# Performance work log

Measured on AMD Instinct MI355X. Metric: run time of the kernel, lower is better.

Reference implementation:

```python
import jax, jax.numpy as jnp
import numpy as np

T = 5       # Newton-Schulz iterations
EPS = 1e-5


def setup_inputs() -> dict:
    key = jax.random.key(0)
    k1, k2 = jax.random.split(key)
    N, F = 500000, 128
    X = jax.random.normal(k1, (N, F), dtype=jnp.float32)
    # running_rot buffer: random orthogonal rotation (eye at init; use QR for a non-trivial one)
    M = jax.random.normal(k2, (1, F, F), dtype=jnp.float32)
    Q, _ = jnp.linalg.qr(M)
    return {"X": X, "running_rot": Q.astype(jnp.float32)}


def _whiten(X):
    # iterative_normalization_py.forward, training path, g=1 group
    x = X.T[None]                              # [g=1, d, m]
    d, m = x.shape[1], x.shape[2]
    mean = jnp.mean(x, axis=-1, keepdims=True)
    xc = x - mean                              # centered [1, d, m]
    I = jnp.eye(d, dtype=X.dtype)[None]
    # Sigma = eps*I + xc xc^T / m  (baddbmm with beta=eps, alpha=1/m)
    Sigma = EPS * I + jnp.einsum('gdm,gem->gde', xc, xc) / m
    rTr = 1.0 / jnp.trace(Sigma, axis1=1, axis2=2)[:, None, None]  # 1/tr(Sigma)
    Sn = Sigma * rTr                           # trace-normalized covariance
    P = I
    for _ in range(T):                         # P_{k+1} = 1.5 P_k - 0.5 P_k^3 Sn
        P = 1.5 * P - 0.5 * (P @ P @ P @ Sn)
    wm = P * jnp.sqrt(rTr)                     # whitening matrix = Sigma^{-1/2} (approx)
    xn = wm @ xc                               # [1, d, m]
    return xn[0].T                             # back to [N, F]


def reference(X, running_rot):
    Xn = _whiten(X)                            # [N, F]
    # X_hat = einsum('bgc,gdc->bgd', X_hat, running_rot) with g=1
    out = jnp.einsum('nc,dc->nd', Xn, running_rot[0])
    return out
```

## Files before the change

### kernel.cpp

```cpp
#include <hip/hip_runtime.h>
#include <math.h>

#define NROWS  500000
#define NCHK   7813
#define EPSV   1e-5f

typedef __bf16 bf16_t;
typedef __bf16 bf16x4 __attribute__((ext_vector_type(4)));
typedef __bf16 bf16x8 __attribute__((ext_vector_type(8)));
typedef float  f32x4  __attribute__((ext_vector_type(4)));

static const size_t GT_OFF   = 131072;
static const size_t WB_OFF   = 327680;
static const size_t MEAN_OFF = 360448;
static const size_t BIAS_OFF = 360960;
static const size_t CS_OFF   = 393216;
static const size_t GRAM_OFF = 1048576;

__global__ __launch_bounds__(256) void k_stats(const float* __restrict__ X,
        float* __restrict__ csPart, float* __restrict__ gramPart) {
    __shared__ bf16_t sxtT[2][8192];
    __shared__ float  scs[256][4];
    const int t    = threadIdx.x;
    const int lane = t & 63;
    const int w    = t >> 6;
    const int oct  = t >> 5;
    const int fg4  = t & 31;
    const int cl   = lane & 15;
    const int kq   = lane >> 4;
    const int G    = gridDim.x;

    f32x4 acc[2][8];
    #pragma unroll
    for (int a = 0; a < 2; a++)
        #pragma unroll
        for (int b = 0; b < 8; b++)
            acc[a][b] = (f32x4){0.f, 0.f, 0.f, 0.f};
    float cs0 = 0.f, cs1 = 0.f, cs2 = 0.f, cs3 = 0.f;

    f32x4 R[8];

    auto KF = [](int f) { return (f ^ (f >> 3)) & 7; };

    auto GLOADC = [&](int ch) {
        const size_t row0 = (size_t)ch << 6;
        #pragma unroll
        for (int i = 0; i < 8; i++) {
            const size_t row = row0 + oct * 8 + i;
            R[i] = (row < NROWS)
                 ? *reinterpret_cast<const f32x4*>(X + row * 128 + fg4 * 4)
                 : (f32x4){0.f, 0.f, 0.f, 0.f};
        }
    };
    auto DSWRITEC = [&](int buf) {
        #pragma unroll
        for (int i = 0; i < 8; i++) {
            cs0 += R[i][0]; cs1 += R[i][1]; cs2 += R[i][2]; cs3 += R[i][3];
        }
        bf16_t* S = sxtT[buf];
        #pragma unroll
        for (int j = 0; j < 4; j++) {
            const int f = fg4 * 4 + j;
            const int g = oct ^ KF(f);
            bf16x8 v;
            #pragma unroll
            for (int i = 0; i < 8; i++) v[i] = (bf16_t)R[i][j];
            *reinterpret_cast<bf16x8*>(&S[f * 64 + g * 8]) = v;
        }
    };
    auto MFMAC = [&](int buf) {
        const bf16_t* S = sxtT[buf];
        #pragma unroll
        for (int kb = 0; kb < 2; kb++) {
            const int gq = kb * 4 + kq;
            bf16x8 fa[2];
            #pragma unroll
            for (int a = 0; a < 2; a++) {
                const int f = (w * 2 + a) * 16 + cl;
                fa[a] = *reinterpret_cast<const bf16x8*>(&S[f * 64 + ((gq ^ KF(f)) << 3)]);
            }
            #pragma unroll
            for (int b = 0; b < 8; b++) {
                const int f = b * 16 + cl;
                const bf16x8 fb = *reinterpret_cast<const bf16x8*>(&S[f * 64 + ((gq ^ KF(f)) << 3)]);
                acc[0][b] = __builtin_amdgcn_mfma_f32_16x16x32_bf16(fa[0], fb, acc[0][b], 0, 0, 0);
                acc[1][b] = __builtin_amdgcn_mfma_f32_16x16x32_bf16(fa[1], fb, acc[1][b], 0, 0, 0);
            }
        }
    };

    int ch0 = blockIdx.x;
    GLOADC(ch0);
    DSWRITEC(0);
    __syncthreads();
    for (;;) {
        const int ch1 = ch0 + G;
        const bool v1 = ch1 < NCHK;
        if (v1) GLOADC(ch1);
        MFMAC(0);
        if (v1) DSWRITEC(1);
        __syncthreads();
        if (!v1) break;
        const int ch2 = ch1 + G;
        const bool v2 = ch2 < NCHK;
        if (v2) GLOADC(ch2);
        MFMAC(1);
        if (v2) DSWRITEC(0);
        __syncthreads();
        if (!v2) break;
        ch0 = ch2;
    }

    float* gp = gramPart + (size_t)blockIdx.x * 16384;
    #pragma unroll
    for (int a = 0; a < 2; a++)
        #pragma unroll
        for (int b = 0; b < 8; b++) {
            const int col  = b * 16 + cl;
            const int row0 = (w * 2 + a) * 16 + kq * 4;
            __builtin_nontemporal_store(acc[a][b],
                reinterpret_cast<f32x4*>(&gp[col * 128 + row0]));
        }
    scs[t][0] = cs0; scs[t][1] = cs1; scs[t][2] = cs2; scs[t][3] = cs3;
    __syncthreads();
    if (t < 128) {
        float s = 0.f;
        #pragma unroll
        for (int q = 0; q < 8; q++) s += scs[q * 32 + (t >> 2)][t & 3];
        csPart[(size_t)blockIdx.x * 128 + t] = s;
    }
}

__global__ __launch_bounds__(256) void k_gred(const float* __restrict__ gramPart,
        const float* __restrict__ csPart, float* __restrict__ gramTot,
        float* __restrict__ mean, int G) {
    const int t = threadIdx.x;
    const int b = blockIdx.x;
    if (b == 256) {
        if (t < 128) {
            float s = 0.f;
            int g = 0;
            for (; g + 8 <= G; g += 8) {
                float p[8];
                #pragma unroll
                for (int u = 0; u < 8; u++) p[u] = csPart[(size_t)(g + u) * 128 + t];
                s += ((p[0] + p[1]) + (p[2] + p[3])) + ((p[4] + p[5]) + (p[6] + p[7]));
            }
            for (; g < G; g++) s += csPart[(size_t)g * 128 + t];
            mean[t] = s * (1.0f / (float)NROWS);
        }
        return;
    }
    const int e  = b * 64 + (t & 63);
    const int sl = t >> 6;
    float s = 0.f;
    int g = sl;
    for (; g + 28 < G; g += 32) {
        float v[8];
        #pragma unroll
        for (int u = 0; u < 8; u++)
            v[u] = __builtin_nontemporal_load(&gramPart[(size_t)(g + 4 * u) * 16384 + e]);
        s += ((v[0] + v[1]) + (v[2] + v[3])) + ((v[4] + v[5]) + (v[6] + v[7]));
    }
    for (; g < G; g += 4)
        s += __builtin_nontemporal_load(&gramPart[(size_t)g * 16384 + e]);
    __shared__ float red[4][64];
    red[sl][t & 63] = s;
    __syncthreads();
    if (t < 64)
        gramTot[b * 64 + t] = (red[0][t] + red[1][t]) + (red[2][t] + red[3][t]);
}

__global__ __launch_bounds__(256) void k_ns(const float* __restrict__ gramTot,
        const float* __restrict__ mean, const float* __restrict__ Rg,
        bf16_t* __restrict__ Wb, float* __restrict__ bias) {
    __shared__ bf16_t sPh[16384], sPl[16384], sSn[16384], sTT[16384];
    const int t = threadIdx.x;
    const int w = t >> 6, lane = t & 63;
    const int cl = lane & 15, kq = lane >> 4;

    float* rs = reinterpret_cast<float*>(sTT);
    float dv = 0.f;
    if (t < 128) {
        const float m = mean[t];
        dv = gramTot[t * 129] * (1.0f / (float)NROWS) - m * m + EPSV;
    }
    rs[t] = dv;
    __syncthreads();
    #pragma unroll
    for (int off = 128; off > 0; off >>= 1) {
        if (t < off) rs[t] += rs[t + off];
        __syncthreads();
    }
    const float rTr = 1.0f / rs[0];
    __syncthreads();
    for (int i = 0; i < 64; i++) {
        const int e = t + (i << 8);
        const int r = e >> 7, c = e & 127;
        float s = gramTot[e] * (1.0f / (float)NROWS) - mean[r] * mean[c];
        if (r == c) s += EPSV;
        const int ix = r * 128 + (c ^ ((r & 7) << 3));
        const float snv = s * rTr;
        sSn[ix] = (bf16_t)snv;
        const float p0 = ((r == c) ? 1.5f : 0.f) - 0.5f * snv;
        const bf16_t ph = (bf16_t)p0;
        sPh[ix] = ph;
        sPl[ix] = (bf16_t)(p0 - (float)ph);
    }
    __syncthreads();

    f32x4 acc[2][8];
    auto NSMM = [&](const bf16_t* __restrict__ Bm) {
        #pragma unroll
        for (int a = 0; a < 2; a++)
            #pragma unroll
            for (int ct = 0; ct < 8; ct++) acc[a][ct] = (f32x4){0.f, 0.f, 0.f, 0.f};
        #pragma unroll
        for (int kb = 0; kb < 4; kb++) {
            const int k0 = kb * 32 + kq * 8;
            bf16x8 ah[2], al[2];
            #pragma unroll
            for (int a = 0; a < 2; a++) {
                const int ra = w * 32 + a * 16 + cl;
                const int ia = ra * 128 + (k0 ^ ((ra & 7) << 3));
                ah[a] = *reinterpret_cast<const bf16x8*>(&sPh[ia]);
                al[a] = *reinterpret_cast<const bf16x8*>(&sPl[ia]);
            }
            #pragma unroll
            for (int ct = 0; ct < 8; ct++) {
                const int rb = ct * 16 + cl;
                const bf16x8 bb = *reinterpret_cast<const bf16x8*>(
                    &Bm[rb * 128 + (k0 ^ ((rb & 7) << 3))]);
                acc[0][ct] = __builtin_amdgcn_mfma_f32_16x16x32_bf16(ah[0], bb, acc[0][ct], 0, 0, 0);
                acc[0][ct] = __builtin_amdgcn_mfma_f32_16x16x32_bf16(al[0], bb, acc[0][ct], 0, 0, 0);
                acc[1][ct] = __builtin_amdgcn_mfma_f32_16x16x32_bf16(ah[1], bb, acc[1][ct], 0, 0, 0);
                acc[1][ct] = __builtin_amdgcn_mfma_f32_16x16x32_bf16(al[1], bb, acc[1][ct], 0, 0, 0);
            }
        }
    };
    auto WRT = [&](bf16_t* __restrict__ D) {
        #pragma unroll
        for (int a = 0; a < 2; a++) {
            const int ro0 = w * 32 + a * 16 + kq * 4;
            #pragma unroll
            for (int ct = 0; ct < 8; ct++) {
                const int co = ct * 16 + cl;
                bf16x4 v = { (bf16_t)acc[a][ct][0], (bf16_t)acc[a][ct][1],
                             (bf16_t)acc[a][ct][2], (bf16_t)acc[a][ct][3] };
                *reinterpret_cast<bf16x4*>(&D[co * 128 + (ro0 ^ ((co & 7) << 3))]) = v;
            }
        }
    };

    for (int it = 0; it < 4; it++) {
        NSMM(sSn);
        WRT(sTT);
        __syncthreads();
        NSMM(sTT);
        __syncthreads();
        WRT(sTT);
        __syncthreads();
        NSMM(sTT);
        #pragma unroll
        for (int a = 0; a < 2; a++) {
            const int ro0 = w * 32 + a * 16 + kq * 4;
            #pragma unroll
            for (int ct = 0; ct < 8; ct++) {
                const int co = ct * 16 + cl;
                const int ix = co * 128 + (ro0 ^ ((co & 7) << 3));
                bf16x4 ph4 = *reinterpret_cast<const bf16x4*>(&sPh[ix]);
                bf16x4 pl4 = *reinterpret_cast<const bf16x4*>(&sPl[ix]);
                bf16x4 nh, nl;
                #pragma unroll
                for (int r = 0; r < 4; r++) {
                    const float pold = (float)ph4[r] + (float)pl4[r];
                    const float pn = 1.5f * pold - 0.5f * acc[a][ct][r];
                    nh[r] = (bf16_t)pn;
                    nl[r] = (bf16_t)(pn - (float)nh[r]);
                }
                *reinterpret_cast<bf16x4*>(&sPh[ix]) = nh;
                *reinterpret_cast<bf16x4*>(&sPl[ix]) = nl;
            }
        }
        __syncthreads();
    }

    const float scal = sqrtf(rTr);
    #pragma unroll
    for (int a = 0; a < 2; a++)
        #pragma unroll
        for (int ct = 0; ct < 8; ct++) acc[a][ct] = (f32x4){0.f, 0.f, 0.f, 0.f};
    #pragma unroll
    for (int kb = 0; kb < 4; kb++) {
        const int k0 = kb * 32 + kq * 8;
        bf16x8 ah[2], al[2];
        #pragma unroll
        for (int a = 0; a < 2; a++) {
            const int ra = w * 32 + a * 16 + cl;
            const float4 rv0 = *reinterpret_cast<const float4*>(&Rg[ra * 128 + k0]);
            const float4 rv1 = *reinterpret_cast<const float4*>(&Rg[ra * 128 + k0 + 4]);
            const float rv[8] = {rv0.x, rv0.y, rv0.z, rv0.w, rv1.x, rv1.y, rv1.z, rv1.w};
            bf16x8 h, l;
            #pragma unroll
            for (int j = 0; j < 8; j++) {
                h[j] = (bf16_t)rv[j];
                l[j] = (bf16_t)(rv[j] - (float)h[j]);
            }
            ah[a] = h; al[a] = l;
        }
        #pragma unroll
        for (int ct = 0; ct < 8; ct++) {
            const int rb = ct * 16 + cl;
            const int ib = rb * 128 + (k0 ^ ((rb & 7) << 3));
            const bf16x8 bh = *reinterpret_cast<const bf16x8*>(&sPh[ib]);
            const bf16x8 bl = *reinterpret_cast<const bf16x8*>(&sPl[ib]);
            #pragma unroll
            for (int a = 0; a < 2; a++) {
                acc[a][ct] = __builtin_amdgcn_mfma_f32_16x16x32_bf16(ah[a], bh, acc[a][ct], 0, 0, 0);
                acc[a][ct] = __builtin_amdgcn_mfma_f32_16x16x32_bf16(al[a], bh, acc[a][ct], 0, 0, 0);
                acc[a][ct] = __builtin_amdgcn_mfma_f32_16x16x32_bf16(ah[a], bl, acc[a][ct], 0, 0, 0);
            }
        }
    }
    #pragma unroll
    for (int a = 0; a < 2; a++) {
        float pb[4] = {0.f, 0.f, 0.f, 0.f};
        #pragma unroll
        for (int ct = 0; ct < 8; ct++) {
            const float mv = mean[ct * 16 + cl];
            #pragma unroll
            for (int r = 0; r < 4; r++) {
                const float wv = acc[a][ct][r] * scal;
                Wb[(w * 32 + a * 16 + kq * 4 + r) * 128 + ct * 16 + cl] = (bf16_t)wv;
                pb[r] += wv * mv;
            }
        }
        #pragma unroll
        for (int r = 0; r < 4; r++) {
            float v = pb[r];
            v += __shfl_xor(v, 1);
            v += __shfl_xor(v, 2);
            v += __shfl_xor(v, 4);
            v += __shfl_xor(v, 8);
            if (cl == 0) bias[w * 32 + a * 16 + kq * 4 + r] = v;
        }
    }
}

__global__ __launch_bounds__(256, 4) void k_out(const float* __restrict__ X,
        const bf16_t* __restrict__ Wb, const float* __restrict__ bias,
        float* __restrict__ out) {
    __shared__ bf16_t sW[128][136];
    __shared__ float sBias[128];
    const int t = threadIdx.x;
    const int w = t >> 6, lane = t & 63;
    const int cl = lane & 15, kq = lane >> 4;
    const int G = gridDim.x;

    float4 A0[8], A1[8];

    auto GLOAD = [&](int tl, float4 (&B)[8]) {
        const size_t rowb = (size_t)tl * 64 + (size_t)w * 16;
        const bool v = rowb < NROWS;
        const float* xr = X + (rowb + cl) * 128;
        #pragma unroll
        for (int kb = 0; kb < 4; kb++) {
            B[2*kb]   = v ? *reinterpret_cast<const float4*>(xr + kb*32 + kq*8)
                          : float4{0.f,0.f,0.f,0.f};
            B[2*kb+1] = v ? *reinterpret_cast<const float4*>(xr + kb*32 + kq*8 + 4)
                          : float4{0.f,0.f,0.f,0.f};
        }
    };
    auto COMPSTORE = [&](int tl, const float4 (&B)[8]) {
        const size_t rowbase = (size_t)tl * 64 + (size_t)w * 16;
        if (rowbase >= NROWS) return;
        bf16x8 xh[4], xl[4];
        #pragma unroll
        for (int kb = 0; kb < 4; kb++) {
            const float4 v0 = B[2*kb], v1 = B[2*kb+1];
            const float xv[8] = {v0.x, v0.y, v0.z, v0.w, v1.x, v1.y, v1.z, v1.w};
            bf16x8 h, l;
            #pragma unroll
            for (int j = 0; j < 8; j++) {
                h[j] = (bf16_t)xv[j];
                l[j] = (bf16_t)(xv[j] - (float)h[j]);
            }
            xh[kb] = h; xl[kb] = l;
        }
        float* orow = out + (rowbase + cl) * 128;
        #pragma unroll
        for (int ct = 0; ct < 8; ct++) {
            f32x4 acc = (f32x4){0.f, 0.f, 0.f, 0.f};
            const int d = ct * 16 + cl;
            #pragma unroll
            for (int kb = 0; kb < 4; kb++) {
                const bf16x8 wf = *reinterpret_cast<const bf16x8*>(&sW[d][kb*32 + kq*8]);
                acc = __builtin_amdgcn_mfma_f32_16x16x32_bf16(wf, xl[kb], acc, 0, 0, 0);
                acc = __builtin_amdgcn_mfma_f32_16x16x32_bf16(wf, xh[kb], acc, 0, 0, 0);
            }
            const f32x4 bv = *reinterpret_cast<const f32x4*>(&sBias[ct * 16 + kq * 4]);
            const f32x4 o = acc - bv;
            __builtin_nontemporal_store(o,
                reinterpret_cast<f32x4*>(&orow[ct * 16 + kq * 4]));
        }
    };

    int t0 = blockIdx.x;
    GLOAD(t0, A0);
    #pragma unroll
    for (int i = 0; i < 8; i++) {
        const int idx = (t + (i << 8)) << 3;
        *reinterpret_cast<bf16x8*>(&sW[idx >> 7][idx & 127]) =
            *reinterpret_cast<const bf16x8*>(&Wb[idx]);
    }
    if (t < 128) sBias[t] = bias[t];
    __syncthreads();
    for (;;) {
        const int t1 = t0 + G;
        if (t1 < NCHK) GLOAD(t1, A1);
        COMPSTORE(t0, A0);
        if (t1 >= NCHK) break;
        const int t2 = t1 + G;
        if (t2 < NCHK) GLOAD(t2, A0);
        COMPSTORE(t1, A1);
        if (t2 >= NCHK) break;
        t0 = t2;
    }
}

extern "C" void kernel_launch(void* const* d_in, const int* in_sizes, int n_in,
                              void* d_out, int out_size, void* d_ws, size_t ws_size,
                              hipStream_t stream) {
    const float* X = (const float*)d_in[0];
    const float* R = (const float*)d_in[1];
    float* out = (float*)d_out;
    char* ws = (char*)d_ws;
    float*  gramTot = (float*)(ws + GT_OFF);
    bf16_t* Wb      = (bf16_t*)(ws + WB_OFF);
    float*  mean    = (float*)(ws + MEAN_OFF);
    float*  bias    = (float*)(ws + BIAS_OFF);
    float*  csPart  = (float*)(ws + CS_OFF);

    int G = 512;
    size_t avail = (ws_size > GRAM_OFF) ? (ws_size - GRAM_OFF) : 0;
    if (avail < (size_t)G * 65536) {
        G = (int)(avail / 65536);
        if (G < 1) G = 1;
        if (G > 512) G = 512;
    }
    float* gramPart = (float*)(ws + GRAM_OFF);

    k_stats<<<dim3(G), dim3(256), 0, stream>>>(X, csPart, gramPart);
    k_gred<<<dim3(257), dim3(256), 0, stream>>>(gramPart, csPart, gramTot, mean, G);
    k_ns<<<dim3(1), dim3(256), 0, stream>>>(gramTot, mean, R, Wb, bias);
    k_out<<<dim3(1024), dim3(256), 0, stream>>>(X, Wb, bias, out);
}
```

Measured before the change: 199.6 us.

## Deepen k_stats load prefetch to two chunks and split column-sum reduction

The stats kernel now keeps two register buffers of X rows, so global loads are issued two chunks ahead of the MFMA work instead of one, giving more memory latency hiding. The price is extra register pressure, which could lower occupancy. Separately, the single-block column-sum reduction in k_gred becomes eight partial-sum blocks, and k_ns finishes that reduction into shared-memory means. This shortens the serial tail of the reduction kernel.

```diff
diff --git a/kernel.cpp b/kernel.cpp
--- a/kernel.cpp
+++ b/kernel.cpp
@@ -12,9 +12,9 @@
 
 static const size_t GT_OFF   = 131072;
 static const size_t WB_OFF   = 327680;
-static const size_t MEAN_OFF = 360448;
 static const size_t BIAS_OFF = 360960;
 static const size_t CS_OFF   = 393216;
+static const size_t CS2_OFF  = 786432;
 static const size_t GRAM_OFF = 1048576;
 
 __global__ __launch_bounds__(256) void k_stats(const float* __restrict__ X,
@@ -38,11 +38,11 @@
             acc[a][b] = (f32x4){0.f, 0.f, 0.f, 0.f};
     float cs0 = 0.f, cs1 = 0.f, cs2 = 0.f, cs3 = 0.f;
 
-    f32x4 R[8];
+    f32x4 R0[8], R1[8];
 
     auto KF = [](int f) { return (f ^ (f >> 3)) & 7; };
 
-    auto GLOADC = [&](int ch) {
+    auto GLOADC = [&](int ch, f32x4 (&R)[8]) {
         const size_t row0 = (size_t)ch << 6;
         #pragma unroll
         for (int i = 0; i < 8; i++) {
@@ -52,7 +52,7 @@
                  : (f32x4){0.f, 0.f, 0.f, 0.f};
         }
     };
-    auto DSWRITEC = [&](int buf) {
+    auto DSWRITEC = [&](int buf, const f32x4 (&R)[8]) {
         #pragma unroll
         for (int i = 0; i < 8; i++) {
             cs0 += R[i][0]; cs1 += R[i][1]; cs2 += R[i][2]; cs3 += R[i][3];
@@ -89,26 +89,28 @@
         }
     };
 
-    int ch0 = blockIdx.x;
-    GLOADC(ch0);
-    DSWRITEC(0);
+    int ch = blockIdx.x;
+    GLOADC(ch, R0);
+    if (ch + G < NCHK) GLOADC(ch + G, R1);
+    DSWRITEC(0, R0);
     __syncthreads();
     for (;;) {
-        const int ch1 = ch0 + G;
-        const bool v1 = ch1 < NCHK;
-        if (v1) GLOADC(ch1);
+        const int c1 = ch + G;
+        const bool v1 = c1 < NCHK;
+        const int c2 = ch + 2 * G;
+        const bool v2 = c2 < NCHK;
+        if (v2) GLOADC(c2, R0);
         MFMAC(0);
-        if (v1) DSWRITEC(1);
+        if (v1) DSWRITEC(1, R1);
         __syncthreads();
         if (!v1) break;
-        const int ch2 = ch1 + G;
-        const bool v2 = ch2 < NCHK;
-        if (v2) GLOADC(ch2);
+        const int c3 = ch + 3 * G;
+        if (c3 < NCHK) GLOADC(c3, R1);
         MFMAC(1);
-        if (v2) DSWRITEC(0);
+        if (v2) DSWRITEC(0, R0);
         __syncthreads();
         if (!v2) break;
-        ch0 = ch2;
+        ch = c2;
     }
 
     float* gp = gramPart + (size_t)blockIdx.x * 16384;
@@ -133,21 +135,23 @@
 
 __global__ __launch_bounds__(256) void k_gred(const float* __restrict__ gramPart,
         const float* __restrict__ csPart, float* __restrict__ gramTot,
-        float* __restrict__ mean, int G) {
+        float* __restrict__ csPart2, int G) {
     const int t = threadIdx.x;
     const int b = blockIdx.x;
-    if (b == 256) {
+    if (b >= 256) {
+        const int s = b - 256;
         if (t < 128) {
-            float s = 0.f;
-            int g = 0;
-            for (; g + 8 <= G; g += 8) {
+            float sum = 0.f;
+            int g = s;
+            for (; g + 56 < G; g += 64) {
                 float p[8];
                 #pragma unroll
-                for (int u = 0; u < 8; u++) p[u] = csPart[(size_t)(g + u) * 128 + t];
-                s += ((p[0] + p[1]) + (p[2] + p[3])) + ((p[4] + p[5]) + (p[6] + p[7]));
-            }
-            for (; g < G; g++) s += csPart[(size_t)g * 128 + t];
-            mean[t] = s * (1.0f / (float)NROWS);
+                for (int u = 0; u < 8; u++)
+                    p[u] = csPart[(size_t)(g + 8 * u) * 128 + t];
+                sum += ((p[0] + p[1]) + (p[2] + p[3])) + ((p[4] + p[5]) + (p[6] + p[7]));
+            }
+            for (; g < G; g += 8) sum += csPart[(size_t)g * 128 + t];
+            csPart2[s * 128 + t] = sum;
         }
         return;
     }
@@ -172,17 +176,26 @@
 }
 
 __global__ __launch_bounds__(256) void k_ns(const float* __restrict__ gramTot,
-        const float* __restrict__ mean, const float* __restrict__ Rg,
+        const float* __restrict__ csPart2, const float* __restrict__ Rg,
         bf16_t* __restrict__ Wb, float* __restrict__ bias) {
     __shared__ bf16_t sPh[16384], sPl[16384], sSn[16384], sTT[16384];
+    __shared__ float smean[128];
     const int t = threadIdx.x;
     const int w = t >> 6, lane = t & 63;
     const int cl = lane & 15, kq = lane >> 4;
 
+    if (t < 128) {
+        float m = 0.f;
+        #pragma unroll
+        for (int s = 0; s < 8; s++) m += csPart2[s * 128 + t];
+        smean[t] = m * (1.0f / (float)NROWS);
+    }
+    __syncthreads();
+
     float* rs = reinterpret_cast<float*>(sTT);
     float dv = 0.f;
     if (t < 128) {
-        const float m = mean[t];
+        const float m = smean[t];
         dv = gramTot[t * 129] * (1.0f / (float)NROWS) - m * m + EPSV;
     }
     rs[t] = dv;
@@ -197,7 +210,7 @@
     for (int i = 0; i < 64; i++) {
         const int e = t + (i << 8);
         const int r = e >> 7, c = e & 127;
-        float s = gramTot[e] * (1.0f / (float)NROWS) - mean[r] * mean[c];
+        float s = gramTot[e] * (1.0f / (float)NROWS) - smean[r] * smean[c];
         if (r == c) s += EPSV;
         const int ix = r * 128 + (c ^ ((r & 7) << 3));
         const float snv = s * rTr;
@@ -327,7 +340,7 @@
         float pb[4] = {0.f, 0.f, 0.f, 0.f};
         #pragma unroll
         for (int ct = 0; ct < 8; ct++) {
-            const float mv = mean[ct * 16 + cl];
+            const float mv = smean[ct * 16 + cl];
             #pragma unroll
             for (int r = 0; r < 4; r++) {
                 const float wv = acc[a][ct][r] * scal;
@@ -437,9 +450,9 @@
     char* ws = (char*)d_ws;
     float*  gramTot = (float*)(ws + GT_OFF);
     bf16_t* Wb      = (bf16_t*)(ws + WB_OFF);
-    float*  mean    = (float*)(ws + MEAN_OFF);
     float*  bias    = (float*)(ws + BIAS_OFF);
     float*  csPart  = (float*)(ws + CS_OFF);
+    float*  csPart2 = (float*)(ws + CS2_OFF);
 
     int G = 512;
     size_t avail = (ws_size > GRAM_OFF) ? (ws_size - GRAM_OFF) : 0;
@@ -451,7 +464,7 @@
     float* gramPart = (float*)(ws + GRAM_OFF);
 
     k_stats<<<dim3(G), dim3(256), 0, stream>>>(X, csPart, gramPart);
-    k_gred<<<dim3(257), dim3(256), 0, stream>>>(gramPart, csPart, gramTot, mean, G);
-    k_ns<<<dim3(1), dim3(256), 0, stream>>>(gramTot, mean, R, Wb, bias);
+    k_gred<<<dim3(264), dim3(256), 0, stream>>>(gramPart, csPart, gramTot, csPart2, G);
+    k_ns<<<dim3(1), dim3(256), 0, stream>>>(gramTot, csPart2, R, Wb, bias);
     k_out<<<dim3(1024), dim3(256), 0, stream>>>(X, Wb, bias, out);
 }
```

Result: slower. 204.1 us (+2.3%).
